# Kernel tuning notes

Hardware: AMD Instinct MI355X
Metric: run time of the kernel (lower is better)

## Reference

```python
import jax, jax.numpy as jnp
import numpy as np

D_MODEL = 1024
NUM_HEADS = 16
D_HEAD = D_MODEL // NUM_HEADS


def setup_inputs() -> dict:
    key = jax.random.key(0)
    kx, kq, kk, kv, ko = jax.random.split(key, 5)
    b, seq = 4, 2048
    x = jax.random.normal(kx, (b, seq, D_MODEL), dtype=jnp.float32)
    # Original uses ones for q/k/v and randn for output; use small random weights
    # for a numerically meaningful baseline of the same math.
    Wq = jax.random.normal(kq, (D_MODEL, D_MODEL), dtype=jnp.float32) * 0.02
    Wk = jax.random.normal(kk, (D_MODEL, D_MODEL), dtype=jnp.float32) * 0.02
    Wv = jax.random.normal(kv, (D_MODEL, D_MODEL), dtype=jnp.float32) * 0.02
    Wo = jax.random.normal(ko, (D_MODEL, D_MODEL), dtype=jnp.float32) * 0.02
    return {"x": x, "Wq": Wq, "Wk": Wk, "Wv": Wv, "Wo": Wo}


def reference(x, Wq, Wk, Wv, Wo):
    b, seq, d = x.shape
    h, dh = NUM_HEADS, D_HEAD

    def split_heads(t):  # [b, s, d] -> [b, h, s, dh]
        return t.reshape(b, seq, h, dh).transpose(0, 2, 1, 3)

    q = split_heads(x @ Wq.T)
    k = split_heads(x @ Wk.T)
    v = split_heads(x @ Wv.T)

    scores = jnp.einsum('bhqd,bhkd->bhqk', q, k) / jnp.sqrt(jnp.float32(dh))
    causal = jnp.tril(jnp.ones((seq, seq), dtype=bool))
    scores = jnp.where(causal, scores, -jnp.inf)
    attn = jax.nn.softmax(scores, axis=-1)
    out = jnp.einsum('bhqk,bhkd->bhqd', attn, v)  # [b, h, s, dh]
    out = out.transpose(0, 2, 1, 3).reshape(b, seq, d)
    return out @ Wo.T
```

## Files before the change

kernel.cpp:

```cpp
#include <hip/hip_runtime.h>
#include <stdint.h>

typedef unsigned short u16;
typedef __attribute__((ext_vector_type(8))) __bf16 bf16x8;
typedef __attribute__((ext_vector_type(4))) float f32x4;

#define AS1 __attribute__((address_space(1)))
#define AS3 __attribute__((address_space(3)))
#define LOG2E 1.4426950408889634f

#define BAR() __builtin_amdgcn_s_barrier()
#define VMC6() asm volatile("s_waitcnt vmcnt(6)" ::: "memory")
#define VMC0() asm volatile("s_waitcnt vmcnt(0)" ::: "memory")

__device__ __forceinline__ u16 f2bf(float f) {
    union { __bf16 h; u16 u; } cv;
    cv.h = (__bf16)f;
    return cv.u;
}

__device__ __forceinline__ float vmax4(f32x4 x) {
    return fmaxf(fmaxf(x[0], x[1]), fmaxf(x[2], x[3]));
}
__device__ __forceinline__ float vsum4(f32x4 x) {
    return (x[0] + x[1]) + (x[2] + x[3]);
}

__global__ __launch_bounds__(256) void cvt_kernel(
    const float* __restrict__ src, u16* __restrict__ dst, int n8)
{
    int i = blockIdx.x * 256 + threadIdx.x;
    if (i >= n8) return;
    const float4* s = (const float4*)src;
    float4 f0 = s[(size_t)i * 2], f1 = s[(size_t)i * 2 + 1];
    ushort4 a, b;
    a.x = f2bf(f0.x); a.y = f2bf(f0.y); a.z = f2bf(f0.z); a.w = f2bf(f0.w);
    b.x = f2bf(f1.x); b.y = f2bf(f1.y); b.z = f2bf(f1.z); b.w = f2bf(f1.w);
    ((ushort4*)dst)[(size_t)i * 2]     = a;
    ((ushort4*)dst)[(size_t)i * 2 + 1] = b;
}

__global__ __launch_bounds__(256) void cvt3_kernel(
    const float* __restrict__ wq, const float* __restrict__ wk,
    const float* __restrict__ wv, u16* __restrict__ dst)
{
    int i = blockIdx.x * 256 + threadIdx.x;
    int seg = i >> 17;
    const float* s = (seg == 0) ? wq : (seg == 1) ? wk : wv;
    float sc = (seg == 0) ? 0.125f : 1.0f;
    int j = i & 131071;
    const float4* sp = (const float4*)s;
    float4 f0 = sp[(size_t)j * 2], f1 = sp[(size_t)j * 2 + 1];
    ushort4 a, b;
    a.x = f2bf(f0.x * sc); a.y = f2bf(f0.y * sc); a.z = f2bf(f0.z * sc); a.w = f2bf(f0.w * sc);
    b.x = f2bf(f1.x * sc); b.y = f2bf(f1.y * sc); b.z = f2bf(f1.z * sc); b.w = f2bf(f1.w * sc);
    ((ushort4*)dst)[(size_t)i * 2]     = a;
    ((ushort4*)dst)[(size_t)i * 2 + 1] = b;
}

#define LDS_OFF(p, h) ((((p) * 4 + (h)) * 8192))

__device__ __forceinline__ void stage_A(
    const u16* __restrict__ G, int kt, int hm, u16* region, int t)
{
    int w6 = t & ~63;
#pragma unroll
    for (int i = 0; i < 2; ++i) {
        int s = i * 512 + t;
        int r = s >> 3;
        int j = (s & 7) ^ (r & 7);
        int row = (r & 63) + ((r >> 6) << 7) + (hm << 6);
        const u16* g = G + (size_t)row * 1024 + kt * 64 + j * 8;
        u16* lp = region + (i * 512 + w6) * 8;
        __builtin_amdgcn_global_load_lds((AS1 unsigned int*)g, (AS3 unsigned int*)lp, 16, 0, 0);
    }
}

__device__ __forceinline__ void stage_B(
    const u16* __restrict__ G, int kt, int hb, u16* region, int t)
{
    int w6 = t & ~63;
#pragma unroll
    for (int i = 0; i < 2; ++i) {
        int s = i * 512 + t;
        int r = s >> 3;
        int j = (s & 7) ^ (r & 7);
        int row = hb * 128 + r;
        const u16* g = G + (size_t)row * 1024 + kt * 64 + j * 8;
        u16* lp = region + (i * 512 + w6) * 8;
        __builtin_amdgcn_global_load_lds((AS1 unsigned int*)g, (AS3 unsigned int*)lp, 16, 0, 0);
    }
}

__device__ __forceinline__ bf16x8 fragr(const u16* region, int row, int j) {
    int byte = row * 128 + ((j ^ (row & 7)) << 4);
    return *(const bf16x8*)((const char*)region + byte);
}

__global__ __launch_bounds__(512, 2) void gemm_qkv_256(
    const u16* __restrict__ X, const u16* __restrict__ W3, u16* __restrict__ QKV)
{
    __shared__ __attribute__((aligned(16))) u16 lds[65536];

    const int t  = threadIdx.x;
    const int l  = t & 63, w = t >> 6;
    const int wm = w >> 2, wn = w & 3;
    const int lr = l & 15, lg = l >> 4;

    int bid = (int)blockIdx.x;
    int wg  = (bid & 7) * 48 + (bid >> 3);
    int mx  = wg / 12, ny = wg % 12;
    const int mb = mx * 256, nb = ny * 256;
    const u16* A = X  + (size_t)mb * 1024;
    const u16* B = W3 + (size_t)nb * 1024;

    const int NT = 16;

    stage_A(A, 0, 0, lds + LDS_OFF(0, 0), t);
    stage_B(B, 0, 0, lds + LDS_OFF(0, 2), t);
    stage_B(B, 0, 1, lds + LDS_OFF(0, 3), t);
    stage_A(A, 0, 1, lds + LDS_OFF(0, 1), t);
    stage_A(A, 1, 0, lds + LDS_OFF(1, 0), t);
    stage_B(B, 1, 0, lds + LDS_OFF(1, 2), t);
    stage_B(B, 1, 1, lds + LDS_OFF(1, 3), t);
    VMC6();
    BAR();

    f32x4 acc[8][4];
#pragma unroll
    for (int i = 0; i < 8; ++i)
#pragma unroll
        for (int j = 0; j < 4; ++j) acc[i][j] = f32x4{0.f, 0.f, 0.f, 0.f};

    for (int kt = 0; kt < NT; ++kt) {
        const int p = kt & 1;
        u16* A0r = lds + LDS_OFF(p, 0);
        u16* A1r = lds + LDS_OFF(p, 1);
        u16* B0r = lds + LDS_OFF(p, 2);
        u16* B1r = lds + LDS_OFF(p, 3);
        u16* A1n = lds + LDS_OFF(p ^ 1, 1);
        const u16* Bw = (wn >= 2) ? B1r : B0r;
        const int brow0 = (wn & 1) * 64;

        bf16x8 af[4][2], bf[4][2];

#pragma unroll
        for (int mi = 0; mi < 4; ++mi)
#pragma unroll
            for (int ks = 0; ks < 2; ++ks)
                af[mi][ks] = fragr(A0r, wm * 64 + mi * 16 + lr, ks * 4 + lg);
#pragma unroll
        for (int ni = 0; ni < 2; ++ni)
#pragma unroll
            for (int ks = 0; ks < 2; ++ks)
                bf[ni][ks] = fragr(Bw, brow0 + ni * 16 + lr, ks * 4 + lg);
        if (kt + 1 < NT) stage_A(A, kt + 1, 1, A1n, t);
        BAR();
        __builtin_amdgcn_s_setprio(1);
#pragma unroll
        for (int mi = 0; mi < 4; ++mi)
#pragma unroll
            for (int ni = 0; ni < 2; ++ni)
#pragma unroll
                for (int ks = 0; ks < 2; ++ks)
                    acc[mi][ni] = __builtin_amdgcn_mfma_f32_16x16x32_bf16(af[mi][ks], bf[ni][ks], acc[mi][ni], 0, 0, 0);
        __builtin_amdgcn_s_setprio(0);
        BAR();

#pragma unroll
        for (int ni = 2; ni < 4; ++ni)
#pragma unroll
            for (int ks = 0; ks < 2; ++ks)
                bf[ni][ks] = fragr(Bw, brow0 + ni * 16 + lr, ks * 4 + lg);
        if (kt + 2 < NT) stage_A(A, kt + 2, 0, A0r, t);
        BAR();
        __builtin_amdgcn_s_setprio(1);
#pragma unroll
        for (int mi = 0; mi < 4; ++mi)
#pragma unroll
            for (int ni = 2; ni < 4; ++ni)
#pragma unroll
                for (int ks = 0; ks < 2; ++ks)
                    acc[mi][ni] = __builtin_amdgcn_mfma_f32_16x16x32_bf16(af[mi][ks], bf[ni][ks], acc[mi][ni], 0, 0, 0);
        __builtin_amdgcn_s_setprio(0);
        BAR();

#pragma unroll
        for (int mi = 0; mi < 4; ++mi)
#pragma unroll
            for (int ks = 0; ks < 2; ++ks)
                af[mi][ks] = fragr(A1r, wm * 64 + mi * 16 + lr, ks * 4 + lg);
        if (kt + 2 < NT) stage_B(B, kt + 2, 0, B0r, t);
        BAR();
        __builtin_amdgcn_s_setprio(1);
#pragma unroll
        for (int mi = 0; mi < 4; ++mi)
#pragma unroll
            for (int ni = 0; ni < 2; ++ni)
#pragma unroll
                for (int ks = 0; ks < 2; ++ks)
                    acc[4 + mi][ni] = __builtin_amdgcn_mfma_f32_16x16x32_bf16(af[mi][ks], bf[ni][ks], acc[4 + mi][ni], 0, 0, 0);
        __builtin_amdgcn_s_setprio(0);
        BAR();

        if (kt + 2 < NT) {
            stage_B(B, kt + 2, 1, B1r, t);
            VMC6();
        } else if (kt + 1 < NT) {
            VMC0();
        }
        BAR();
        __builtin_amdgcn_s_setprio(1);
#pragma unroll
        for (int mi = 0; mi < 4; ++mi)
#pragma unroll
            for (int ni = 2; ni < 4; ++ni)
#pragma unroll
                for (int ks = 0; ks < 2; ++ks)
                    acc[4 + mi][ni] = __builtin_amdgcn_mfma_f32_16x16x32_bf16(af[mi][ks], bf[ni][ks], acc[4 + mi][ni], 0, 0, 0);
        __builtin_amdgcn_s_setprio(0);
        BAR();
    }

#pragma unroll
    for (int mi = 0; mi < 8; ++mi)
#pragma unroll
        for (int ni = 0; ni < 4; ++ni) {
            int col = nb + wn * 64 + ni * 16 + lr;
#pragma unroll
            for (int v = 0; v < 4; ++v) {
                int row = mb + wm * 128 + mi * 16 + lg * 4 + v;
                QKV[(size_t)row * 3072 + col] = f2bf(acc[mi][ni][v]);
            }
        }
}

__device__ __forceinline__ void gemm_tile_body_f32(
    const u16* __restrict__ A, const u16* __restrict__ B, float* __restrict__ Cp,
    int K, int ldc, int mb, int nb, u16* As, u16* Bs)
{
    const int t  = threadIdx.x;
    const int l  = t & 63, w = t >> 6;
    const int wm = w >> 1, wn = w & 1;
    const int lr = l & 15, lg = l >> 4;

    f32x4 acc[4][4];
#pragma unroll
    for (int i = 0; i < 4; ++i)
#pragma unroll
        for (int j = 0; j < 4; ++j) acc[i][j] = f32x4{0.f, 0.f, 0.f, 0.f};

    for (int k0 = 0; k0 < K; k0 += 32) {
        __syncthreads();
#pragma unroll
        for (int i = 0; i < 2; ++i) {
            int chunk = i * 256 + t;
            int row   = chunk >> 2;
            int c8    = (chunk & 3) << 3;
            const u16* ga = A + (size_t)(mb + row) * K + k0 + c8;
            const u16* gb = B + (size_t)(nb + row) * K + k0 + c8;
            u16* la = As + (i * 256 + w * 64) * 8;
            u16* lb = Bs + (i * 256 + w * 64) * 8;
            __builtin_amdgcn_global_load_lds((AS1 unsigned int*)ga, (AS3 unsigned int*)la, 16, 0, 0);
            __builtin_amdgcn_global_load_lds((AS1 unsigned int*)gb, (AS3 unsigned int*)lb, 16, 0, 0);
        }
        __syncthreads();
        bf16x8 af[4], bfr[4];
#pragma unroll
        for (int mi = 0; mi < 4; ++mi)
            af[mi] = *(const bf16x8*)(As + (wm * 64 + mi * 16 + lr) * 32 + lg * 8);
#pragma unroll
        for (int ni = 0; ni < 4; ++ni)
            bfr[ni] = *(const bf16x8*)(Bs + (wn * 64 + ni * 16 + lr) * 32 + lg * 8);
#pragma unroll
        for (int mi = 0; mi < 4; ++mi)
#pragma unroll
            for (int ni = 0; ni < 4; ++ni)
                acc[mi][ni] = __builtin_amdgcn_mfma_f32_16x16x32_bf16(af[mi], bfr[ni], acc[mi][ni], 0, 0, 0);
    }
#pragma unroll
    for (int mi = 0; mi < 4; ++mi)
#pragma unroll
        for (int ni = 0; ni < 4; ++ni) {
            int col = nb + wn * 64 + ni * 16 + lr;
#pragma unroll
            for (int v = 0; v < 4; ++v) {
                int row = mb + wm * 64 + mi * 16 + lg * 4 + v;
                Cp[(size_t)row * ldc + col] = acc[mi][ni][v];
            }
        }
}

__global__ __launch_bounds__(256, 2) void gemm_out_kernel(
    const u16* __restrict__ A, const u16* __restrict__ B, float* __restrict__ C)
{
    __shared__ __attribute__((aligned(16))) u16 As[128 * 32];
    __shared__ __attribute__((aligned(16))) u16 Bs[128 * 32];
    int bid = (int)blockIdx.x + (int)gridDim.x * (int)blockIdx.y;
    int wg  = (bid & 7) * 64 + (bid >> 3);
    int mx  = wg >> 3;
    int my  = wg & 7;
    gemm_tile_body_f32(A, B, C, 1024, 1024, mx * 128, my * 128, As, Bs);
}

#define SEQ  2048
#define PSTR 72
#define NQT  16

__device__ __forceinline__ void attn_qtile(
    const u16* __restrict__ Qg, const u16* __restrict__ Kg, const u16* __restrict__ Vg,
    u16* __restrict__ outp, int b, int h, int qt,
    u16* QP, u16* Ks, u16* Vt)
{
    const int t  = threadIdx.x;
    const int l  = t & 63, w = t >> 6;
    const int lr = l & 15, lg = l >> 4;
    const int q0 = qt * 128;
    const int sr = t >> 3;
    const int sc = (t & 7) << 3;
    const int vswz = sc;

    __syncthreads();
#pragma unroll
    for (int i = 0; i < 4; ++i) {
        int r = sr + i * 32;
        *(uint4*)(QP + r * PSTR + sc) = *(const uint4*)(Qg + (size_t)(q0 + r) * 3072 + sc);
    }
    __syncthreads();
    bf16x8 qf[2][2];
#pragma unroll
    for (int mi = 0; mi < 2; ++mi)
#pragma unroll
        for (int ks = 0; ks < 2; ++ks)
            qf[mi][ks] = *(const bf16x8*)(QP + (w * 32 + mi * 16 + lr) * PSTR + ks * 32 + lg * 8);

    uint4 kpf[2], vpf[2];
#pragma unroll
    for (int i = 0; i < 2; ++i) {
        int r = sr + i * 32;
        kpf[i] = *(const uint4*)(Kg + (size_t)r * 3072 + sc);
        vpf[i] = *(const uint4*)(Vg + (size_t)r * 3072 + sc);
    }

    f32x4 o[4][2];
#pragma unroll
    for (int nd = 0; nd < 4; ++nd)
#pragma unroll
        for (int mi = 0; mi < 2; ++mi) o[nd][mi] = f32x4{0.f, 0.f, 0.f, 0.f};
    float mrow[2]  = { -__builtin_inff(), -__builtin_inff() };
    float mrowL[2] = { -__builtin_inff(), -__builtin_inff() };
    float lrow[2]  = { 0.f, 0.f };

    const int nkt = 2 * qt + 2;
    for (int kt = 0; kt < nkt; ++kt) {
        const int k0 = kt * 64;
        __syncthreads();
#pragma unroll
        for (int i = 0; i < 2; ++i) {
            int r = sr + i * 32;
            *(uint4*)(Ks + r * PSTR + sc) = kpf[i];
            int rs = r ^ vswz;
            union { uint4 q; u16 u[8]; } uv; uv.q = vpf[i];
#pragma unroll
            for (int j = 0; j < 8; ++j)
                Vt[(sc + j) * PSTR + rs] = uv.u[j];
        }
        if (kt + 1 < nkt) {
            const int k0n = k0 + 64;
#pragma unroll
            for (int i = 0; i < 2; ++i) {
                int r = sr + i * 32;
                kpf[i] = *(const uint4*)(Kg + (size_t)(k0n + r) * 3072 + sc);
                vpf[i] = *(const uint4*)(Vg + (size_t)(k0n + r) * 3072 + sc);
            }
        }
        __syncthreads();

        f32x4 s[4][2];
#pragma unroll
        for (int ni = 0; ni < 4; ++ni)
#pragma unroll
            for (int mi = 0; mi < 2; ++mi) s[ni][mi] = f32x4{0.f, 0.f, 0.f, 0.f};
        __builtin_amdgcn_s_setprio(1);
#pragma unroll
        for (int ks = 0; ks < 2; ++ks) {
            bf16x8 kb[4];
#pragma unroll
            for (int ni = 0; ni < 4; ++ni)
                kb[ni] = *(const bf16x8*)(Ks + (ni * 16 + lr) * PSTR + ks * 32 + lg * 8);
#pragma unroll
            for (int ni = 0; ni < 4; ++ni)
#pragma unroll
                for (int mi = 0; mi < 2; ++mi)
                    s[ni][mi] = __builtin_amdgcn_mfma_f32_16x16x32_bf16(kb[ni], qf[mi][ks], s[ni][mi], 0, 0, 0);
        }
        __builtin_amdgcn_s_setprio(0);

#pragma unroll
        for (int mi = 0; mi < 2; ++mi) {
            if ((k0 + 63) > (q0 + w * 32 + mi * 16)) {
                int qpos = q0 + w * 32 + mi * 16 + lr;
#pragma unroll
                for (int ni = 0; ni < 4; ++ni) {
                    int kb0 = k0 + ni * 16 + lg * 4;
#pragma unroll
                    for (int v = 0; v < 4; ++v)
                        if (kb0 + v > qpos) s[ni][mi][v] = -__builtin_inff();
                }
            }
        }

        float rmax[2];
        bool grew = false;
#pragma unroll
        for (int mi = 0; mi < 2; ++mi) {
            float r = fmaxf(fmaxf(vmax4(s[0][mi]), vmax4(s[1][mi])),
                            fmaxf(vmax4(s[2][mi]), vmax4(s[3][mi])));
            r = fmaxf(r, __shfl_xor(r, 16));
            r = fmaxf(r, __shfl_xor(r, 32));
            rmax[mi] = r;
            grew |= (r > mrow[mi]);
        }
        if (__ballot(grew)) {
#pragma unroll
            for (int mi = 0; mi < 2; ++mi) {
                float mn  = fmaxf(mrow[mi], rmax[mi]);
                float mnL = mn * LOG2E;
                float al  = __builtin_amdgcn_exp2f(mrowL[mi] - mnL);
                mrow[mi]  = mn;
                mrowL[mi] = mnL;
                lrow[mi] *= al;
#pragma unroll
                for (int nd = 0; nd < 4; ++nd)
#pragma unroll
                    for (int v = 0; v < 4; ++v) o[nd][mi][v] *= al;
            }
        }
#pragma unroll
        for (int mi = 0; mi < 2; ++mi) {
            float nmL = -mrowL[mi];
#pragma unroll
            for (int ni = 0; ni < 4; ++ni)
#pragma unroll
                for (int v = 0; v < 4; ++v)
                    s[ni][mi][v] = __builtin_amdgcn_exp2f(
                        __builtin_fmaf(s[ni][mi][v], LOG2E, nmL));
            float sum = (vsum4(s[0][mi]) + vsum4(s[1][mi]))
                      + (vsum4(s[2][mi]) + vsum4(s[3][mi]));
            sum += __shfl_xor(sum, 16);
            sum += __shfl_xor(sum, 32);
            lrow[mi] += sum;
            int prow = (w * 32 + mi * 16 + lr) * PSTR + lg * 4;
#pragma unroll
            for (int ni = 0; ni < 4; ++ni) {
                ushort4 u;
                u.x = f2bf(s[ni][mi][0]); u.y = f2bf(s[ni][mi][1]);
                u.z = f2bf(s[ni][mi][2]); u.w = f2bf(s[ni][mi][3]);
                *(ushort4*)(QP + prow + ni * 16) = u;
            }
        }

        __builtin_amdgcn_s_setprio(1);
#pragma unroll
        for (int ks = 0; ks < 2; ++ks) {
            bf16x8 pa[2], vb[4];
#pragma unroll
            for (int mi = 0; mi < 2; ++mi)
                pa[mi] = *(const bf16x8*)(QP + (w * 32 + mi * 16 + lr) * PSTR + ks * 32 + lg * 8);
#pragma unroll
            for (int nd = 0; nd < 4; ++nd) {
                int d = nd * 16 + lr;
                vb[nd] = *(const bf16x8*)(Vt + d * PSTR + ((ks * 32 + lg * 8) ^ (((d >> 3) & 7) << 3)));
            }
#pragma unroll
            for (int nd = 0; nd < 4; ++nd)
#pragma unroll
                for (int mi = 0; mi < 2; ++mi)
                    o[nd][mi] = __builtin_amdgcn_mfma_f32_16x16x32_bf16(vb[nd], pa[mi], o[nd][mi], 0, 0, 0);
        }
        __builtin_amdgcn_s_setprio(0);
    }

#pragma unroll
    for (int mi = 0; mi < 2; ++mi) {
        float inv = 1.f / lrow[mi];
        int row = q0 + w * 32 + mi * 16 + lr;
        u16* op = outp + (size_t)(b * SEQ + row) * 1024 + h * 64 + lg * 4;
#pragma unroll
        for (int nd = 0; nd < 4; ++nd) {
            ushort4 u;
            u.x = f2bf(o[nd][mi][0] * inv); u.y = f2bf(o[nd][mi][1] * inv);
            u.z = f2bf(o[nd][mi][2] * inv); u.w = f2bf(o[nd][mi][3] * inv);
            *(ushort4*)(op + nd * 16) = u;
        }
    }
}

__global__ __launch_bounds__(256, 2) void attn_kernel(
    const u16* __restrict__ qkv, u16* __restrict__ outp)
{
    __shared__ __attribute__((aligned(16))) u16 QP[128 * PSTR];
    __shared__ __attribute__((aligned(16))) u16 Ks[64 * PSTR];
    __shared__ __attribute__((aligned(16))) u16 Vt[64 * PSTR];

    const int bid = (int)blockIdx.x + (int)blockIdx.y * 8;
    const int xcd = bid & 7;
    const int j   = bid >> 3;
    const int bh  = xcd * 8 + (j & 7);
    const int qp  = j >> 3;
    const int b   = bh >> 4, h = bh & 15;

    const u16* Qg = qkv + (size_t)b * SEQ * 3072 + h * 64;
    const u16* Kg = Qg + 1024;
    const u16* Vg = Qg + 2048;

    attn_qtile(Qg, Kg, Vg, outp, b, h, qp,           QP, Ks, Vt);
    attn_qtile(Qg, Kg, Vg, outp, b, h, NQT - 1 - qp, QP, Ks, Vt);
}

extern "C" void kernel_launch(void* const* d_in, const int* in_sizes, int n_in,
                              void* d_out, int out_size, void* d_ws, size_t ws_size,
                              hipStream_t stream)
{
    (void)in_sizes; (void)n_in; (void)out_size; (void)ws_size;
    const float* x  = (const float*)d_in[0];
    const float* Wq = (const float*)d_in[1];
    const float* Wk = (const float*)d_in[2];
    const float* Wv = (const float*)d_in[3];
    const float* Wo = (const float*)d_in[4];

    u16*   qkv = (u16*)d_ws;
    u16*   xb  = qkv + (size_t)8192 * 3072;
    u16*   att = xb;
    u16*   w3  = (u16*)d_out;
    u16*   wob = qkv;
    float* out = (float*)d_out;

    cvt_kernel <<<dim3(4096), 256, 0, stream>>>(x, xb, 1048576);
    cvt3_kernel<<<dim3(1536), 256, 0, stream>>>(Wq, Wk, Wv, w3);

    gemm_qkv_256<<<dim3(384), 512, 0, stream>>>(xb, w3, qkv);
    attn_kernel <<<dim3(8, 64), 256, 0, stream>>>(qkv, att);

    cvt_kernel<<<dim3(512), 256, 0, stream>>>(Wo, wob, 131072);
    gemm_out_kernel<<<dim3(64, 8), 256, 0, stream>>>(att, wob, out);
}
```

Measured before the change: 273.4 us.

## Double-buffer attention K/V tiles and stage GEMM epilogues through LDS

The attention loop now keeps two K and two V^T shared-memory buffers. It commits the next tile while computing on the current one, which drops one of the two barriers per iteration. Both GEMM epilogues now stage accumulators in LDS and write coalesced 16-byte rows to global memory, replacing scattered 2- and 4-byte stores. This adds LDS use in attention, which may affect occupancy, and adds extra barriers in the epilogues.

```diff
diff --git a/kernel.cpp b/kernel.cpp
--- a/kernel.cpp
+++ b/kernel.cpp
@@ -222,23 +222,34 @@
         BAR();
     }
 
-#pragma unroll
-    for (int mi = 0; mi < 8; ++mi)
-#pragma unroll
-        for (int ni = 0; ni < 4; ++ni) {
-            int col = nb + wn * 64 + ni * 16 + lr;
-#pragma unroll
-            for (int v = 0; v < 4; ++v) {
-                int row = mb + wm * 128 + mi * 16 + lg * 4 + v;
-                QKV[(size_t)row * 3072 + col] = f2bf(acc[mi][ni][v]);
-            }
-        }
+    u16* ep = lds;
+#pragma unroll
+    for (int mi = 0; mi < 8; ++mi) {
+#pragma unroll
+        for (int ni = 0; ni < 4; ++ni)
+#pragma unroll
+            for (int v = 0; v < 4; ++v)
+                ep[(wm * 16 + lg * 4 + v) * 264 + wn * 64 + ni * 16 + lr] = f2bf(acc[mi][ni][v]);
+        BAR();
+#pragma unroll
+        for (int c = 0; c < 2; ++c) {
+            int ch = c * 512 + t;
+            int srow = ch >> 5, col8 = (ch & 31) << 3;
+            int grow = mb + ((srow >> 4) << 7) + mi * 16 + (srow & 15);
+            *(uint4*)(QKV + (size_t)grow * 3072 + nb + col8) =
+                *(const uint4*)(ep + srow * 264 + col8);
+        }
+        BAR();
+    }
 }
 
 __device__ __forceinline__ void gemm_tile_body_f32(
     const u16* __restrict__ A, const u16* __restrict__ B, float* __restrict__ Cp,
-    int K, int ldc, int mb, int nb, u16* As, u16* Bs)
-{
+    int K, int ldc, int mb, int nb, u16* sh)
+{
+    u16* As = sh;
+    u16* Bs = sh + 128 * 32;
+
     const int t  = threadIdx.x;
     const int l  = t & 63, w = t >> 6;
     const int wm = w >> 1, wn = w & 1;
@@ -278,39 +289,76 @@
             for (int ni = 0; ni < 4; ++ni)
                 acc[mi][ni] = __builtin_amdgcn_mfma_f32_16x16x32_bf16(af[mi], bfr[ni], acc[mi][ni], 0, 0, 0);
     }
-#pragma unroll
-    for (int mi = 0; mi < 4; ++mi)
-#pragma unroll
-        for (int ni = 0; ni < 4; ++ni) {
-            int col = nb + wn * 64 + ni * 16 + lr;
-#pragma unroll
-            for (int v = 0; v < 4; ++v) {
-                int row = mb + wm * 64 + mi * 16 + lg * 4 + v;
-                Cp[(size_t)row * ldc + col] = acc[mi][ni][v];
-            }
-        }
+
+    __syncthreads();
+    float* epf = (float*)sh;
+#pragma unroll
+    for (int s = 0; s < 8; ++s) {
+        int wmS = s >> 2, miS = s & 3;
+        if (wm == wmS) {
+#pragma unroll
+            for (int ni = 0; ni < 4; ++ni)
+#pragma unroll
+                for (int v = 0; v < 4; ++v)
+                    epf[(lg * 4 + v) * 132 + wn * 64 + ni * 16 + lr] = acc[miS][ni][v];
+        }
+        __syncthreads();
+#pragma unroll
+        for (int c = 0; c < 2; ++c) {
+            int ch = c * 256 + t;
+            int srow = ch >> 5, c4 = (ch & 31) << 2;
+            *(float4*)(Cp + (size_t)(mb + wmS * 64 + miS * 16 + srow) * ldc + nb + c4) =
+                *(const float4*)(epf + srow * 132 + c4);
+        }
+        __syncthreads();
+    }
 }
 
 __global__ __launch_bounds__(256, 2) void gemm_out_kernel(
     const u16* __restrict__ A, const u16* __restrict__ B, float* __restrict__ C)
 {
-    __shared__ __attribute__((aligned(16))) u16 As[128 * 32];
-    __shared__ __attribute__((aligned(16))) u16 Bs[128 * 32];
+    __shared__ __attribute__((aligned(16))) u16 sh[128 * 32 * 2];
     int bid = (int)blockIdx.x + (int)gridDim.x * (int)blockIdx.y;
     int wg  = (bid & 7) * 64 + (bid >> 3);
     int mx  = wg >> 3;
     int my  = wg & 7;
-    gemm_tile_body_f32(A, B, C, 1024, 1024, mx * 128, my * 128, As, Bs);
+    gemm_tile_body_f32(A, B, C, 1024, 1024, mx * 128, my * 128, sh);
 }
 
 #define SEQ  2048
 #define PSTR 72
 #define NQT  16
 
+__device__ __forceinline__ void kv_commit(
+    u16* KD, u16* VD, const uint4* kpf, const uint4* vpf, int sr, int sc)
+{
+#pragma unroll
+    for (int i = 0; i < 2; ++i) {
+        int r = sr + i * 32;
+        *(uint4*)(KD + r * PSTR + sc) = kpf[i];
+        int rs = r ^ sc;
+        union { uint4 q; u16 u[8]; } uv; uv.q = vpf[i];
+#pragma unroll
+        for (int j = 0; j < 8; ++j)
+            VD[(sc + j) * PSTR + rs] = uv.u[j];
+    }
+}
+
+__device__ __forceinline__ void kv_prefetch(
+    uint4* kpf, uint4* vpf, const u16* Kg, const u16* Vg, int k0, int sr, int sc)
+{
+#pragma unroll
+    for (int i = 0; i < 2; ++i) {
+        int r = k0 + sr + i * 32;
+        kpf[i] = *(const uint4*)(Kg + (size_t)r * 3072 + sc);
+        vpf[i] = *(const uint4*)(Vg + (size_t)r * 3072 + sc);
+    }
+}
+
 __device__ __forceinline__ void attn_qtile(
     const u16* __restrict__ Qg, const u16* __restrict__ Kg, const u16* __restrict__ Vg,
     u16* __restrict__ outp, int b, int h, int qt,
-    u16* QP, u16* Ks, u16* Vt)
+    u16* QP, u16* Ks0, u16* Ks1, u16* Vt0, u16* Vt1)
 {
     const int t  = threadIdx.x;
     const int l  = t & 63, w = t >> 6;
@@ -318,7 +366,6 @@
     const int q0 = qt * 128;
     const int sr = t >> 3;
     const int sc = (t & 7) << 3;
-    const int vswz = sc;
 
     __syncthreads();
 #pragma unroll
@@ -334,13 +381,12 @@
         for (int ks = 0; ks < 2; ++ks)
             qf[mi][ks] = *(const bf16x8*)(QP + (w * 32 + mi * 16 + lr) * PSTR + ks * 32 + lg * 8);
 
+    const int nkt = 2 * qt + 2;
     uint4 kpf[2], vpf[2];
-#pragma unroll
-    for (int i = 0; i < 2; ++i) {
-        int r = sr + i * 32;
-        kpf[i] = *(const uint4*)(Kg + (size_t)r * 3072 + sc);
-        vpf[i] = *(const uint4*)(Vg + (size_t)r * 3072 + sc);
-    }
+    kv_prefetch(kpf, vpf, Kg, Vg, 0, sr, sc);
+    kv_commit(Ks0, Vt0, kpf, vpf, sr, sc);
+    if (nkt > 1) kv_prefetch(kpf, vpf, Kg, Vg, 64, sr, sc);
+    __syncthreads();
 
     f32x4 o[4][2];
 #pragma unroll
@@ -351,30 +397,17 @@
     float mrowL[2] = { -__builtin_inff(), -__builtin_inff() };
     float lrow[2]  = { 0.f, 0.f };
 
-    const int nkt = 2 * qt + 2;
     for (int kt = 0; kt < nkt; ++kt) {
         const int k0 = kt * 64;
-        __syncthreads();
-#pragma unroll
-        for (int i = 0; i < 2; ++i) {
-            int r = sr + i * 32;
-            *(uint4*)(Ks + r * PSTR + sc) = kpf[i];
-            int rs = r ^ vswz;
-            union { uint4 q; u16 u[8]; } uv; uv.q = vpf[i];
-#pragma unroll
-            for (int j = 0; j < 8; ++j)
-                Vt[(sc + j) * PSTR + rs] = uv.u[j];
-        }
+        u16* Ksc = (kt & 1) ? Ks1 : Ks0;
+        u16* Vtc = (kt & 1) ? Vt1 : Vt0;
+        u16* Ksn = (kt & 1) ? Ks0 : Ks1;
+        u16* Vtn = (kt & 1) ? Vt0 : Vt1;
+
         if (kt + 1 < nkt) {
-            const int k0n = k0 + 64;
-#pragma unroll
-            for (int i = 0; i < 2; ++i) {
-                int r = sr + i * 32;
-                kpf[i] = *(const uint4*)(Kg + (size_t)(k0n + r) * 3072 + sc);
-                vpf[i] = *(const uint4*)(Vg + (size_t)(k0n + r) * 3072 + sc);
-            }
-        }
-        __syncthreads();
+            kv_commit(Ksn, Vtn, kpf, vpf, sr, sc);
+            if (kt + 2 < nkt) kv_prefetch(kpf, vpf, Kg, Vg, k0 + 128, sr, sc);
+        }
 
         f32x4 s[4][2];
 #pragma unroll
@@ -387,7 +420,7 @@
             bf16x8 kb[4];
 #pragma unroll
             for (int ni = 0; ni < 4; ++ni)
-                kb[ni] = *(const bf16x8*)(Ks + (ni * 16 + lr) * PSTR + ks * 32 + lg * 8);
+                kb[ni] = *(const bf16x8*)(Ksc + (ni * 16 + lr) * PSTR + ks * 32 + lg * 8);
 #pragma unroll
             for (int ni = 0; ni < 4; ++ni)
 #pragma unroll
@@ -470,7 +503,7 @@
 #pragma unroll
             for (int nd = 0; nd < 4; ++nd) {
                 int d = nd * 16 + lr;
-                vb[nd] = *(const bf16x8*)(Vt + d * PSTR + ((ks * 32 + lg * 8) ^ (((d >> 3) & 7) << 3)));
+                vb[nd] = *(const bf16x8*)(Vtc + d * PSTR + ((ks * 32 + lg * 8) ^ (((d >> 3) & 7) << 3)));
             }
 #pragma unroll
             for (int nd = 0; nd < 4; ++nd)
@@ -479,6 +512,8 @@
                     o[nd][mi] = __builtin_amdgcn_mfma_f32_16x16x32_bf16(vb[nd], pa[mi], o[nd][mi], 0, 0, 0);
         }
         __builtin_amdgcn_s_setprio(0);
+
+        __syncthreads();
     }
 
 #pragma unroll
@@ -500,8 +535,10 @@
     const u16* __restrict__ qkv, u16* __restrict__ outp)
 {
     __shared__ __attribute__((aligned(16))) u16 QP[128 * PSTR];
-    __shared__ __attribute__((aligned(16))) u16 Ks[64 * PSTR];
-    __shared__ __attribute__((aligned(16))) u16 Vt[64 * PSTR];
+    __shared__ __attribute__((aligned(16))) u16 Ks0[64 * PSTR];
+    __shared__ __attribute__((aligned(16))) u16 Ks1[64 * PSTR];
+    __shared__ __attribute__((aligned(16))) u16 Vt0[64 * PSTR];
+    __shared__ __attribute__((aligned(16))) u16 Vt1[64 * PSTR];
 
     const int bid = (int)blockIdx.x + (int)blockIdx.y * 8;
     const int xcd = bid & 7;
@@ -514,8 +551,8 @@
     const u16* Kg = Qg + 1024;
     const u16* Vg = Qg + 2048;
 
-    attn_qtile(Qg, Kg, Vg, outp, b, h, qp,           QP, Ks, Vt);
-    attn_qtile(Qg, Kg, Vg, outp, b, h, NQT - 1 - qp, QP, Ks, Vt);
+    attn_qtile(Qg, Kg, Vg, outp, b, h, qp,           QP, Ks0, Ks1, Vt0, Vt1);
+    attn_qtile(Qg, Kg, Vg, outp, b, h, NQT - 1 - qp, QP, Ks0, Ks1, Vt0, Vt1);
 }
 
 extern "C" void kernel_launch(void* const* d_in, const int* in_sizes, int n_in,
```

Measured after the change: 285.8 us. 4.5% more time.

## Retile QKV GEMM to 256x192 tiles and stage epilogues through LDS

Applied to the files above, without the earlier changes.

The QKV projection GEMM moves from 256x256 to 256x192 output tiles. That raises the grid from 384 to 512 workgroups, which fills the 256 CUs more evenly, and shrinks the LDS double buffer and accumulator registers. The B staging is split into a two-chunk part and a one-chunk part, with the vmcnt wait retuned to match. Both the QKV GEMM and the output-projection GEMM now write results through LDS and emit coalesced 16-byte row stores instead of scattered per-element stores. This adds extra barriers and LDS traffic in the epilogue, and each tile does less work per load of A.

```diff
diff --git a/kernel.cpp b/kernel.cpp
--- a/kernel.cpp
+++ b/kernel.cpp
@@ -10,7 +10,7 @@
 #define LOG2E 1.4426950408889634f
 
 #define BAR() __builtin_amdgcn_s_barrier()
-#define VMC6() asm volatile("s_waitcnt vmcnt(6)" ::: "memory")
+#define VMC5() asm volatile("s_waitcnt vmcnt(5)" ::: "memory")
 #define VMC0() asm volatile("s_waitcnt vmcnt(0)" ::: "memory")
 
 __device__ __forceinline__ u16 f2bf(float f) {
@@ -58,7 +58,7 @@
     ((ushort4*)dst)[(size_t)i * 2 + 1] = b;
 }
 
-#define LDS_OFF(p, h) ((((p) * 4 + (h)) * 8192))
+#define QBUF 28672
 
 __device__ __forceinline__ void stage_A(
     const u16* __restrict__ G, int kt, int hm, u16* region, int t)
@@ -76,8 +76,8 @@
     }
 }
 
-__device__ __forceinline__ void stage_B(
-    const u16* __restrict__ G, int kt, int hb, u16* region, int t)
+__device__ __forceinline__ void stage_B01(
+    const u16* __restrict__ G, int kt, u16* region, int t)
 {
     int w6 = t & ~63;
 #pragma unroll
@@ -85,11 +85,20 @@
         int s = i * 512 + t;
         int r = s >> 3;
         int j = (s & 7) ^ (r & 7);
-        int row = hb * 128 + r;
-        const u16* g = G + (size_t)row * 1024 + kt * 64 + j * 8;
+        const u16* g = G + (size_t)r * 1024 + kt * 64 + j * 8;
         u16* lp = region + (i * 512 + w6) * 8;
         __builtin_amdgcn_global_load_lds((AS1 unsigned int*)g, (AS3 unsigned int*)lp, 16, 0, 0);
     }
+}
+
+__device__ __forceinline__ void stage_B2(
+    const u16* __restrict__ G, int kt, u16* region, int t)
+{
+    int r = t >> 3;
+    int j = (t & 7) ^ (r & 7);
+    const u16* g = G + (size_t)(128 + r) * 1024 + kt * 64 + j * 8;
+    u16* lp = region + 8192 + ((t & ~63)) * 8;
+    __builtin_amdgcn_global_load_lds((AS1 unsigned int*)g, (AS3 unsigned int*)lp, 16, 0, 0);
 }
 
 __device__ __forceinline__ bf16x8 fragr(const u16* region, int row, int j) {
@@ -100,7 +109,7 @@
 __global__ __launch_bounds__(512, 2) void gemm_qkv_256(
     const u16* __restrict__ X, const u16* __restrict__ W3, u16* __restrict__ QKV)
 {
-    __shared__ __attribute__((aligned(16))) u16 lds[65536];
+    __shared__ __attribute__((aligned(16))) u16 lds[57344];
 
     const int t  = threadIdx.x;
     const int l  = t & 63, w = t >> 6;
@@ -108,41 +117,41 @@
     const int lr = l & 15, lg = l >> 4;
 
     int bid = (int)blockIdx.x;
-    int wg  = (bid & 7) * 48 + (bid >> 3);
-    int mx  = wg / 12, ny = wg % 12;
-    const int mb = mx * 256, nb = ny * 256;
+    int wg  = (bid & 7) * 64 + (bid >> 3);
+    int mx  = wg >> 4, ny = wg & 15;
+    const int mb = mx * 256, nb = ny * 192;
     const u16* A = X  + (size_t)mb * 1024;
     const u16* B = W3 + (size_t)nb * 1024;
 
     const int NT = 16;
 
-    stage_A(A, 0, 0, lds + LDS_OFF(0, 0), t);
-    stage_B(B, 0, 0, lds + LDS_OFF(0, 2), t);
-    stage_B(B, 0, 1, lds + LDS_OFF(0, 3), t);
-    stage_A(A, 0, 1, lds + LDS_OFF(0, 1), t);
-    stage_A(A, 1, 0, lds + LDS_OFF(1, 0), t);
-    stage_B(B, 1, 0, lds + LDS_OFF(1, 2), t);
-    stage_B(B, 1, 1, lds + LDS_OFF(1, 3), t);
-    VMC6();
+    stage_A  (A, 0, 0, lds + 0,             t);
+    stage_B01(B, 0,    lds + 16384,         t);
+    stage_B2 (B, 0,    lds + 16384,         t);
+    stage_A  (A, 0, 1, lds + 8192,          t);
+    stage_A  (A, 1, 0, lds + QBUF + 0,      t);
+    stage_B01(B, 1,    lds + QBUF + 16384,  t);
+    stage_B2 (B, 1,    lds + QBUF + 16384,  t);
+    VMC5();
     BAR();
 
-    f32x4 acc[8][4];
+    f32x4 acc[8][3];
 #pragma unroll
     for (int i = 0; i < 8; ++i)
 #pragma unroll
-        for (int j = 0; j < 4; ++j) acc[i][j] = f32x4{0.f, 0.f, 0.f, 0.f};
+        for (int j = 0; j < 3; ++j) acc[i][j] = f32x4{0.f, 0.f, 0.f, 0.f};
+
+    const int brow0 = wn * 48;
 
     for (int kt = 0; kt < NT; ++kt) {
         const int p = kt & 1;
-        u16* A0r = lds + LDS_OFF(p, 0);
-        u16* A1r = lds + LDS_OFF(p, 1);
-        u16* B0r = lds + LDS_OFF(p, 2);
-        u16* B1r = lds + LDS_OFF(p, 3);
-        u16* A1n = lds + LDS_OFF(p ^ 1, 1);
-        const u16* Bw = (wn >= 2) ? B1r : B0r;
-        const int brow0 = (wn & 1) * 64;
-
-        bf16x8 af[4][2], bf[4][2];
+        u16* A0r = lds + p * QBUF;
+        u16* A1r = A0r + 8192;
+        u16* Br  = A0r + 16384;
+        u16* A1n = lds + (p ^ 1) * QBUF + 8192;
+        u16* Bn  = lds + p * QBUF + 16384;
+
+        bf16x8 af[4][2], bf[3][2];
 
 #pragma unroll
         for (int mi = 0; mi < 4; ++mi)
@@ -153,7 +162,7 @@
         for (int ni = 0; ni < 2; ++ni)
 #pragma unroll
             for (int ks = 0; ks < 2; ++ks)
-                bf[ni][ks] = fragr(Bw, brow0 + ni * 16 + lr, ks * 4 + lg);
+                bf[ni][ks] = fragr(Br, brow0 + ni * 16 + lr, ks * 4 + lg);
         if (kt + 1 < NT) stage_A(A, kt + 1, 1, A1n, t);
         BAR();
         __builtin_amdgcn_s_setprio(1);
@@ -168,20 +177,16 @@
         BAR();
 
 #pragma unroll
-        for (int ni = 2; ni < 4; ++ni)
+        for (int ks = 0; ks < 2; ++ks)
+            bf[2][ks] = fragr(Br, brow0 + 32 + lr, ks * 4 + lg);
+        if (kt + 2 < NT) stage_A(A, kt + 2, 0, A0r, t);
+        BAR();
+        __builtin_amdgcn_s_setprio(1);
+#pragma unroll
+        for (int mi = 0; mi < 4; ++mi)
 #pragma unroll
             for (int ks = 0; ks < 2; ++ks)
-                bf[ni][ks] = fragr(Bw, brow0 + ni * 16 + lr, ks * 4 + lg);
-        if (kt + 2 < NT) stage_A(A, kt + 2, 0, A0r, t);
-        BAR();
-        __builtin_amdgcn_s_setprio(1);
-#pragma unroll
-        for (int mi = 0; mi < 4; ++mi)
-#pragma unroll
-            for (int ni = 2; ni < 4; ++ni)
-#pragma unroll
-                for (int ks = 0; ks < 2; ++ks)
-                    acc[mi][ni] = __builtin_amdgcn_mfma_f32_16x16x32_bf16(af[mi][ks], bf[ni][ks], acc[mi][ni], 0, 0, 0);
+                acc[mi][2] = __builtin_amdgcn_mfma_f32_16x16x32_bf16(af[mi][ks], bf[2][ks], acc[mi][2], 0, 0, 0);
         __builtin_amdgcn_s_setprio(0);
         BAR();
 
@@ -190,7 +195,7 @@
 #pragma unroll
             for (int ks = 0; ks < 2; ++ks)
                 af[mi][ks] = fragr(A1r, wm * 64 + mi * 16 + lr, ks * 4 + lg);
-        if (kt + 2 < NT) stage_B(B, kt + 2, 0, B0r, t);
+        if (kt + 2 < NT) stage_B01(B, kt + 2, Bn, t);
         BAR();
         __builtin_amdgcn_s_setprio(1);
 #pragma unroll
@@ -204,8 +209,8 @@
         BAR();
 
         if (kt + 2 < NT) {
-            stage_B(B, kt + 2, 1, B1r, t);
-            VMC6();
+            stage_B2(B, kt + 2, Bn, t);
+            VMC5();
         } else if (kt + 1 < NT) {
             VMC0();
         }
@@ -214,31 +219,42 @@
 #pragma unroll
         for (int mi = 0; mi < 4; ++mi)
 #pragma unroll
-            for (int ni = 2; ni < 4; ++ni)
-#pragma unroll
-                for (int ks = 0; ks < 2; ++ks)
-                    acc[4 + mi][ni] = __builtin_amdgcn_mfma_f32_16x16x32_bf16(af[mi][ks], bf[ni][ks], acc[4 + mi][ni], 0, 0, 0);
+            for (int ks = 0; ks < 2; ++ks)
+                acc[4 + mi][2] = __builtin_amdgcn_mfma_f32_16x16x32_bf16(af[mi][ks], bf[2][ks], acc[4 + mi][2], 0, 0, 0);
         __builtin_amdgcn_s_setprio(0);
         BAR();
     }
 
-#pragma unroll
-    for (int mi = 0; mi < 8; ++mi)
-#pragma unroll
-        for (int ni = 0; ni < 4; ++ni) {
-            int col = nb + wn * 64 + ni * 16 + lr;
-#pragma unroll
-            for (int v = 0; v < 4; ++v) {
-                int row = mb + wm * 128 + mi * 16 + lg * 4 + v;
-                QKV[(size_t)row * 3072 + col] = f2bf(acc[mi][ni][v]);
+    u16* ep = lds;
+#pragma unroll
+    for (int mi = 0; mi < 8; ++mi) {
+#pragma unroll
+        for (int ni = 0; ni < 3; ++ni)
+#pragma unroll
+            for (int v = 0; v < 4; ++v)
+                ep[(wm * 16 + lg * 4 + v) * 200 + wn * 48 + ni * 16 + lr] = f2bf(acc[mi][ni][v]);
+        BAR();
+#pragma unroll
+        for (int c = 0; c < 2; ++c) {
+            int ch = c * 512 + t;
+            if (ch < 768) {
+                int srow = ch / 24, col8 = (ch % 24) * 8;
+                int grow = mb + (srow >> 4) * 128 + mi * 16 + (srow & 15);
+                *(uint4*)(QKV + (size_t)grow * 3072 + nb + col8) =
+                    *(const uint4*)(ep + srow * 200 + col8);
             }
         }
+        BAR();
+    }
 }
 
 __device__ __forceinline__ void gemm_tile_body_f32(
     const u16* __restrict__ A, const u16* __restrict__ B, float* __restrict__ Cp,
-    int K, int ldc, int mb, int nb, u16* As, u16* Bs)
-{
+    int K, int ldc, int mb, int nb, u16* sh)
+{
+    u16* As = sh;
+    u16* Bs = sh + 128 * 32;
+
     const int t  = threadIdx.x;
     const int l  = t & 63, w = t >> 6;
     const int wm = w >> 1, wn = w & 1;
@@ -278,29 +294,40 @@
             for (int ni = 0; ni < 4; ++ni)
                 acc[mi][ni] = __builtin_amdgcn_mfma_f32_16x16x32_bf16(af[mi], bfr[ni], acc[mi][ni], 0, 0, 0);
     }
-#pragma unroll
-    for (int mi = 0; mi < 4; ++mi)
-#pragma unroll
-        for (int ni = 0; ni < 4; ++ni) {
-            int col = nb + wn * 64 + ni * 16 + lr;
-#pragma unroll
-            for (int v = 0; v < 4; ++v) {
-                int row = mb + wm * 64 + mi * 16 + lg * 4 + v;
-                Cp[(size_t)row * ldc + col] = acc[mi][ni][v];
-            }
-        }
+
+    __syncthreads();
+    float* epf = (float*)sh;
+#pragma unroll
+    for (int s = 0; s < 8; ++s) {
+        int wmS = s >> 2, miS = s & 3;
+        if (wm == wmS) {
+#pragma unroll
+            for (int ni = 0; ni < 4; ++ni)
+#pragma unroll
+                for (int v = 0; v < 4; ++v)
+                    epf[(lg * 4 + v) * 132 + wn * 64 + ni * 16 + lr] = acc[miS][ni][v];
+        }
+        __syncthreads();
+#pragma unroll
+        for (int c = 0; c < 2; ++c) {
+            int ch = c * 256 + t;
+            int srow = ch >> 5, c4 = (ch & 31) << 2;
+            *(float4*)(Cp + (size_t)(mb + wmS * 64 + miS * 16 + srow) * ldc + nb + c4) =
+                *(const float4*)(epf + srow * 132 + c4);
+        }
+        __syncthreads();
+    }
 }
 
 __global__ __launch_bounds__(256, 2) void gemm_out_kernel(
     const u16* __restrict__ A, const u16* __restrict__ B, float* __restrict__ C)
 {
-    __shared__ __attribute__((aligned(16))) u16 As[128 * 32];
-    __shared__ __attribute__((aligned(16))) u16 Bs[128 * 32];
+    __shared__ __attribute__((aligned(16))) u16 sh[128 * 32 * 2];
     int bid = (int)blockIdx.x + (int)gridDim.x * (int)blockIdx.y;
     int wg  = (bid & 7) * 64 + (bid >> 3);
     int mx  = wg >> 3;
     int my  = wg & 7;
-    gemm_tile_body_f32(A, B, C, 1024, 1024, mx * 128, my * 128, As, Bs);
+    gemm_tile_body_f32(A, B, C, 1024, 1024, mx * 128, my * 128, sh);
 }
 
 #define SEQ  2048
@@ -539,7 +566,7 @@
     cvt_kernel <<<dim3(4096), 256, 0, stream>>>(x, xb, 1048576);
     cvt3_kernel<<<dim3(1536), 256, 0, stream>>>(Wq, Wk, Wv, w3);
 
-    gemm_qkv_256<<<dim3(384), 512, 0, stream>>>(xb, w3, qkv);
+    gemm_qkv_256<<<dim3(512), 512, 0, stream>>>(xb, w3, qkv);
     attn_kernel <<<dim3(8, 64), 256, 0, stream>>>(qkv, att);
 
     cvt_kernel<<<dim3(512), 256, 0, stream>>>(Wo, wob, 131072);
```

Result: no change. 272.5 us (-0.3%).
